# Kernel tuning notes

Hardware: AMD Instinct MI355X
Metric: run time of the kernel (lower is better)

The kernel has to match this reference:

```python
import jax, jax.numpy as jnp
import numpy as np

D_MODEL = 256  # out_channels + skip_channels
D_INNER = 512  # expand * d_model
D_STATE = 16
D_CONV = 4
DT_RANK = 16   # ceil(d_model / 16)


def setup_inputs() -> dict:
    key = jax.random.key(0)
    ks = jax.random.split(key, 16)
    s = 0.05
    inp = {
        "x": jax.random.normal(ks[0], (2, 256, 32, 32), jnp.float32),
        "skip": jax.random.normal(ks[1], (2, 128, 64, 64), jnp.float32),
        # ConvTranspose2d(in=256, out=128, k=2, s=2): torch weight (in, out, kH, kW)
        "up_w": jax.random.normal(ks[2], (256, 128, 2, 2), jnp.float32) * s,
        "up_b": jax.random.normal(ks[3], (128,), jnp.float32) * s,
        # Mamba params
        "in_proj_w": jax.random.normal(ks[4], (2 * D_INNER, D_MODEL), jnp.float32) * s,
        "conv1d_w": jax.random.normal(ks[5], (D_INNER, D_CONV), jnp.float32) * s,
        "conv1d_b": jax.random.normal(ks[6], (D_INNER,), jnp.float32) * s,
        "x_proj_w": jax.random.normal(ks[7], (DT_RANK + 2 * D_STATE, D_INNER), jnp.float32) * s,
        "dt_proj_w": jax.random.normal(ks[8], (D_INNER, DT_RANK), jnp.float32) * s,
        "dt_proj_b": jax.random.normal(ks[9], (D_INNER,), jnp.float32) * s,
        "A_log": jnp.log(jnp.tile(jnp.arange(1, D_STATE + 1, dtype=jnp.float32), (D_INNER, 1))),
        "D": jnp.ones((D_INNER,), jnp.float32),
        "out_proj_w": jax.random.normal(ks[10], (D_MODEL, D_INNER), jnp.float32) * s,
        # Conv2d(256 -> 128, k=3, pad=1) + BN affine
        "conv_w": jax.random.normal(ks[11], (128, 256, 3, 3), jnp.float32) * s,
        "conv_b": jax.random.normal(ks[12], (128,), jnp.float32) * s,
        "bn_gamma": jnp.ones((128,), jnp.float32),
        "bn_beta": jnp.zeros((128,), jnp.float32),
    }
    return inp


def _forward(x, skip, up_w, up_b, in_proj_w, conv1d_w, conv1d_b, x_proj_w,
             dt_proj_w, dt_proj_b, A_log, D, out_proj_w, conv_w, conv_b,
             bn_gamma, bn_beta):
    B, Cin, H, W = x.shape
    # --- ConvTranspose2d k=2, s=2: each input pixel expands to a 2x2 block ---
    up = jnp.einsum('bchw,coxy->bohxwy', x, up_w)  # (B, Cout, H, 2, W, 2)
    Cout = up_w.shape[1]
    up = up.reshape(B, Cout, 2 * H, 2 * W) + up_b[None, :, None, None]
    xc = jnp.concatenate([up, skip], axis=1)  # (B, d_model, 2H, 2W)
    _, d_model, H2, W2 = xc.shape
    L = H2 * W2
    seq = xc.reshape(B, d_model, L).transpose(0, 2, 1)  # (B, L, d_model)

    # --- Mamba block ---
    xz = seq @ in_proj_w.T  # (B, L, 2*d_inner)
    d_inner = in_proj_w.shape[0] // 2
    xi, z = xz[..., :d_inner], xz[..., d_inner:]
    # depthwise causal conv1d along L
    xt = xi.transpose(0, 2, 1)  # (B, d_inner, L)
    d_conv = conv1d_w.shape[-1]
    xt = jnp.pad(xt, ((0, 0), (0, 0), (d_conv - 1, 0)))
    xt = jax.lax.conv_general_dilated(
        xt, conv1d_w[:, None, :], (1,), 'VALID',
        dimension_numbers=('NCH', 'OIH', 'NCH'), feature_group_count=d_inner)
    xt = xt + conv1d_b[None, :, None]
    u = jax.nn.silu(xt.transpose(0, 2, 1))  # (B, L, d_inner)

    d_state = A_log.shape[1]
    dbc = u @ x_proj_w.T  # (B, L, dt_rank + 2*d_state)
    dt_rank = x_proj_w.shape[0] - 2 * d_state
    dt = jax.nn.softplus(dbc[..., :dt_rank] @ dt_proj_w.T + dt_proj_b)  # (B, L, d_inner)
    Bm = dbc[..., dt_rank:dt_rank + d_state]  # (B, L, d_state)
    Cm = dbc[..., dt_rank + d_state:]         # (B, L, d_state)
    A = -jnp.exp(A_log)                       # (d_inner, d_state)

    def step(h, inputs):
        dt_t, B_t, C_t, u_t = inputs  # (B,d_inner),(B,d_state),(B,d_state),(B,d_inner)
        dA = jnp.exp(dt_t[:, :, None] * A)  # (B, d_inner, d_state)
        h = dA * h + (dt_t * u_t)[:, :, None] * B_t[:, None, :]
        y_t = jnp.einsum('bdn,bn->bd', h, C_t)
        return h, y_t

    h0 = jnp.zeros((B, d_inner, d_state), seq.dtype)
    xs = (dt.transpose(1, 0, 2), Bm.transpose(1, 0, 2),
          Cm.transpose(1, 0, 2), u.transpose(1, 0, 2))
    _, ys = jax.lax.scan(step, h0, xs)  # ys: (L, B, d_inner)
    y = ys.transpose(1, 0, 2) + u * D
    y = y * jax.nn.silu(z)
    out = y @ out_proj_w.T  # (B, L, d_model)
    mam = out.transpose(0, 2, 1).reshape(B, d_model, H2, W2)

    # --- residual + Conv3x3 + BatchNorm (training stats) + GELU ---
    xr = xc + mam
    y2 = jax.lax.conv_general_dilated(
        xr, conv_w, (1, 1), ((1, 1), (1, 1)),
        dimension_numbers=('NCHW', 'OIHW', 'NCHW')) + conv_b[None, :, None, None]
    mu = y2.mean(axis=(0, 2, 3), keepdims=True)
    var = y2.var(axis=(0, 2, 3), keepdims=True)
    y2 = (y2 - mu) / jnp.sqrt(var + 1e-5) * bn_gamma[None, :, None, None] + bn_beta[None, :, None, None]
    return jax.nn.gelu(y2, approximate=False)


def reference(x, skip, up_w, up_b, in_proj_w, conv1d_w, conv1d_b, x_proj_w,
              dt_proj_w, dt_proj_b, A_log, D, out_proj_w, conv_w, conv_b,
              bn_gamma, bn_beta):
    return _forward(x, skip, up_w, up_b, in_proj_w, conv1d_w, conv1d_b,
                    x_proj_w, dt_proj_w, dt_proj_b, A_log, D, out_proj_w,
                    conv_w, conv_b, bn_gamma, bn_beta)
```

## Files before the change

kernel.cpp:

```cpp
#include <hip/hip_runtime.h>
#include <hip/hip_bf16.h>
#include <math.h>

typedef __hip_bfloat16 bf16;
typedef __attribute__((ext_vector_type(8))) short s8v;
typedef __attribute__((ext_vector_type(4))) float f4v;

#define NB 2
#define NT 8192
#define NSEG 128
#define SEGLEN 32


__device__ __forceinline__ short f2s(float x){
    bf16 t = __float2bfloat16(x);
    return *reinterpret_cast<short*>(&t);
}
__device__ __forceinline__ float s2f(short s){
    bf16 t = *reinterpret_cast<bf16*>(&s);
    return __bfloat162float(t);
}
__device__ __forceinline__ void powtree(float e1, float* a){
    a[0]=e1;      a[1]=a[0]*a[0];  a[2]=a[1]*a[0];  a[3]=a[1]*a[1];
    a[4]=a[3]*a[0]; a[5]=a[3]*a[1]; a[6]=a[3]*a[2]; a[7]=a[3]*a[3];
    a[8]=a[7]*a[0]; a[9]=a[7]*a[1]; a[10]=a[7]*a[2]; a[11]=a[7]*a[3];
    a[12]=a[7]*a[4]; a[13]=a[7]*a[5]; a[14]=a[7]*a[6]; a[15]=a[7]*a[7];
}

__global__ void k_prep3(const float* __restrict__ inw, const float* __restrict__ outw,
        const float* __restrict__ upw, const float* __restrict__ cvw,
        const float* __restrict__ xpw,
        short* inw_bf, short* outw_bf, short* upw_bf, short* cwt_bf,
        short* xw_bf, float* stats){
    int i = blockIdx.x*256 + threadIdx.x;
    if (i < 262144){ inw_bf[i] = f2s(inw[i]); }
    else if (i < 393216){ int j = i-262144; outw_bf[j] = f2s(outw[j]); }
    else if (i < 524288){
        int j = i-393216; int n = j >> 8, c = j & 255;
        upw_bf[j] = f2s(upw[c*512 + n]);
    }
    else if (i < 819200){
        int j = i-524288; int o = j / 2304, k = j % 2304;
        int p = k >> 8, c = k & 255;
        cwt_bf[j] = f2s(cvw[o*2304 + c*9 + p]);
    }
    else if (i < 851968){
        int j = i-819200; int r = j >> 9;
        xw_bf[j] = (r < 48) ? f2s(xpw[j]) : (short)0;
    }
    else if (i < 852224){ stats[i-851968] = 0.f; }
}

__global__ __launch_bounds__(256) void k_skipT(const float* __restrict__ skip,
        short* __restrict__ xc){
    __shared__ float tile[128][33];
    int bid = blockIdx.x;
    int b = bid >> 7, hw0 = (bid & 127)*32;
    int tid = threadIdx.x;
    int hwl = tid & 31, og = tid >> 5;
    #pragma unroll
    for (int it = 0; it < 16; ++it){
        int o = it*8 + og;
        tile[o][hwl] = skip[((size_t)(b*128 + o))*4096 + hw0 + hwl];
    }
    __syncthreads();
    int tl = tid >> 3, oc = (tid & 7)*16;
    int t = b*4096 + hw0 + tl;
    s8v v0, v1;
    #pragma unroll
    for (int q = 0; q < 8; ++q){
        v0[q] = f2s(tile[oc + q][tl]);
        v1[q] = f2s(tile[oc + 8 + q][tl]);
    }
    *(s8v*)(xc + (size_t)t*256 + 128 + oc)     = v0;
    *(s8v*)(xc + (size_t)t*256 + 128 + oc + 8) = v1;
}

__global__ __launch_bounds__(256) void k_xT(const float* __restrict__ x,
        short* __restrict__ xT){
    __shared__ float tile[32][257];
    int bid = blockIdx.x;
    int b = bid >> 5, p0 = (bid & 31)*32;
    int tid = threadIdx.x;
    int pl = tid & 31, cg = tid >> 5;
    #pragma unroll
    for (int it = 0; it < 32; ++it){
        int c = it*8 + cg;
        tile[pl][c] = x[((size_t)(b*256 + c))*1024 + p0 + pl];
    }
    __syncthreads();
    int pll = tid >> 3, cc = (tid & 7)*32;
    #pragma unroll
    for (int g = 0; g < 4; ++g){
        s8v v;
        #pragma unroll
        for (int q = 0; q < 8; ++q) v[q] = f2s(tile[pll][cc + g*8 + q]);
        *(s8v*)(xT + ((size_t)(b*1024 + p0 + pll))*256 + cc + g*8) = v;
    }
}

__device__ __forceinline__ s8v conv_loadA(const short* __restrict__ xr,
                                          int m, int kabs){
    int p = kabs >> 8, cin = kabs & 255;
    int dy = p/3 - 1, dx = p%3 - 1;
    int hw = m & 4095; int h = hw >> 6, w = hw & 63;
    int hh = h + dy, ww = w + dx;
    s8v v;
    if ((unsigned)hh < 64u && (unsigned)ww < 64u){
        v = *(const s8v*)(xr + (size_t)((m & ~4095) + (hh<<6) + ww)*256 + cin);
    } else {
        #pragma unroll
        for (int q = 0; q < 8; ++q) v[q] = 0;
    }
    return v;
}

template<int MODE>
__global__ __launch_bounds__(256) void k_mfma(const short* __restrict__ A, int lda,
        const short* __restrict__ B, int ldb, int K,
        void* __restrict__ Cd, int ldc, short* __restrict__ R,
        const float* __restrict__ Pf){
    __shared__ __align__(16) short As[128*72];
    __shared__ __align__(16) short Bs[64*72];
    const int tid = threadIdx.x;
    const int m0 = blockIdx.x*128, n0 = blockIdx.y*64;
    const int waveId = tid >> 6, lane = tid & 63;
    const int quad = lane >> 4, l15 = lane & 15;
    int kbase = 0;
    float* psum = nullptr;
    if (MODE == 3){
        kbase = blockIdx.z * 768;
        psum = (float*)Cd + (size_t)blockIdx.z * (8192*128);
    }
    f4v acc[2][4];
    #pragma unroll
    for (int a = 0; a < 2; ++a)
        #pragma unroll
        for (int b = 0; b < 4; ++b)
            acc[a][b] = (f4v){0.f,0.f,0.f,0.f};

    for (int k0 = 0; k0 < K; k0 += 64){
        __syncthreads();
        #pragma unroll
        for (int l = 0; l < 4; ++l){
            int c = tid + l*256;
            int row = c & 127, kq = c >> 7;
            s8v v;
            if (MODE == 3){
                v = conv_loadA(A, m0 + row, kbase + k0 + kq*8);
            } else {
                v = *(const s8v*)(A + (size_t)(m0+row)*lda + k0 + kq*8);
            }
            *(s8v*)&As[row*72 + kq*8] = v;
        }
        #pragma unroll
        for (int l = 0; l < 2; ++l){
            int c = tid + l*256;
            int n = c & 63, kq = c >> 6;
            *(s8v*)&Bs[n*72 + kq*8] =
                *(const s8v*)(B + (size_t)(n0+n)*ldb + kbase + k0 + kq*8);
        }
        __syncthreads();
        #pragma unroll
        for (int ks = 0; ks < 2; ++ks){
            s8v af[2], bfr[4];
            #pragma unroll
            for (int mi = 0; mi < 2; ++mi)
                af[mi] = *(s8v*)&As[(waveId*32 + mi*16 + l15)*72 + ks*32 + quad*8];
            #pragma unroll
            for (int ni = 0; ni < 4; ++ni)
                bfr[ni] = *(s8v*)&Bs[(ni*16 + l15)*72 + ks*32 + quad*8];
            #pragma unroll
            for (int mi = 0; mi < 2; ++mi)
                #pragma unroll
                for (int ni = 0; ni < 4; ++ni)
                    acc[mi][ni] = __builtin_amdgcn_mfma_f32_16x16x32_bf16(
                        af[mi], bfr[ni], acc[mi][ni], 0, 0, 0);
        }
    }
    #pragma unroll
    for (int mi = 0; mi < 2; ++mi){
        #pragma unroll
        for (int ni = 0; ni < 4; ++ni){
            int rowb = m0 + waveId*32 + mi*16 + quad*4;
            int col  = n0 + ni*16 + l15;
            #pragma unroll
            for (int r = 0; r < 4; ++r){
                int m = rowb + r;
                float v = acc[mi][ni][r];
                if (MODE == 2){
                    v += s2f(R[(size_t)m*ldc + col]);
                    ((short*)Cd)[(size_t)m*ldc + col] = f2s(v);
                } else if (MODE == 3){
                    psum[(size_t)m*128 + col] = v;
                } else if (MODE == 5){
                    int b = m >> 10, hp = (m & 1023) >> 5, wp = m & 31;
                    int o = col >> 2, ij = col & 3;
                    int h2 = 2*hp + (ij >> 1), w2 = 2*wp + (ij & 1);
                    int t = b*4096 + h2*64 + w2;
                    ((short*)Cd)[(size_t)t*256 + o] = f2s(v + Pf[o]);
                } else if (MODE == 6){
                    if (col < 512) ((short*)Cd)[(size_t)m*512 + col] = f2s(v);
                    else           R[(size_t)m*512 + col - 512]      = f2s(v);
                }
            }
        }
    }
}

__global__ __launch_bounds__(256) void k_reduce2(const float* __restrict__ psum,
        const float* __restrict__ cvb, float* __restrict__ y2,
        float* __restrict__ stats){
    __shared__ float ls[128], ls2[128];
    int tid = threadIdx.x;
    if (tid < 128){ ls[tid] = 0.f; ls2[tid] = 0.f; }
    __syncthreads();
    int base = blockIdx.x*4096;
    float lacc = 0.f, lacc2 = 0.f;
    int o = 0;
    #pragma unroll
    for (int it = 0; it < 16; ++it){
        int i = base + it*256 + tid;
        o = i & 127;
        float v = psum[i] + psum[i + 1048576] + psum[i + 2097152] + cvb[o];
        y2[i] = v;
        lacc += v; lacc2 += v*v;
    }
    atomicAdd(&ls[o], lacc);
    atomicAdd(&ls2[o], lacc2);
    __syncthreads();
    if (tid < 128){
        atomicAdd(&stats[tid], ls[tid]);
        atomicAdd(&stats[128 + tid], ls2[tid]);
    }
}

__global__ __launch_bounds__(256) void k_xproj32(const short* __restrict__ A,
        const short* __restrict__ B, float* __restrict__ dbc){
    __shared__ __align__(16) short As[2][32*72];
    __shared__ __align__(16) short Bs[2][64*72];
    const int tid = threadIdx.x;
    const int m0 = blockIdx.x*32;
    const int w = tid >> 6, lane = tid & 63;
    const int quad = lane >> 4, l15 = lane & 15;
    const int mi = w & 1, ni = w >> 1;
    const int arow = tid & 31, akq = tid >> 5;
    const int brow = tid & 63, bkq0 = tid >> 6, bkq1 = bkq0 + 4;

    s8v ra  = *(const s8v*)(A + (size_t)(m0+arow)*512 + akq*8);
    s8v rb0 = *(const s8v*)(B + (size_t)brow*512 + bkq0*8);
    s8v rb1 = *(const s8v*)(B + (size_t)brow*512 + bkq1*8);
    *(s8v*)&As[0][arow*72 + akq*8]  = ra;
    *(s8v*)&Bs[0][brow*72 + bkq0*8] = rb0;
    *(s8v*)&Bs[0][brow*72 + bkq1*8] = rb1;
    __syncthreads();

    f4v acc[2];
    acc[0] = (f4v){0.f,0.f,0.f,0.f};
    acc[1] = (f4v){0.f,0.f,0.f,0.f};
    int buf = 0;
    for (int kt = 0; kt < 8; ++kt){
        if (kt + 1 < 8){
            int k0 = (kt+1)*64;
            ra  = *(const s8v*)(A + (size_t)(m0+arow)*512 + k0 + akq*8);
            rb0 = *(const s8v*)(B + (size_t)brow*512 + k0 + bkq0*8);
            rb1 = *(const s8v*)(B + (size_t)brow*512 + k0 + bkq1*8);
        }
        #pragma unroll
        for (int ks = 0; ks < 2; ++ks){
            s8v af = *(s8v*)&As[buf][(mi*16 + l15)*72 + ks*32 + quad*8];
            #pragma unroll
            for (int nf = 0; nf < 2; ++nf){
                s8v bfv = *(s8v*)&Bs[buf][(ni*32 + nf*16 + l15)*72 + ks*32 + quad*8];
                acc[nf] = __builtin_amdgcn_mfma_f32_16x16x32_bf16(af, bfv, acc[nf], 0, 0, 0);
            }
        }
        if (kt + 1 < 8){
            __syncthreads();
            buf ^= 1;
            *(s8v*)&As[buf][arow*72 + akq*8]  = ra;
            *(s8v*)&Bs[buf][brow*72 + bkq0*8] = rb0;
            *(s8v*)&Bs[buf][brow*72 + bkq1*8] = rb1;
            __syncthreads();
        }
    }
    #pragma unroll
    for (int nf = 0; nf < 2; ++nf){
        int col = ni*32 + nf*16 + l15;
        if (col < 48){
            int rowb = m0 + mi*16 + quad*4;
            #pragma unroll
            for (int r = 0; r < 4; ++r)
                dbc[(size_t)(rowb+r)*48 + col] = acc[nf][r];
        }
    }
}

__global__ void k_conv1d(const short* __restrict__ xi, const float* __restrict__ cw,
                         const float* __restrict__ cb, short* __restrict__ u){
    int idx = blockIdx.x*256 + threadIdx.x;
    int t = idx >> 6; int dc = (idx & 63)*8; int l = t & 4095;
    s8v x0 = *(const s8v*)(xi + (size_t)t*512 + dc);
    s8v x1, x2, x3;
    #pragma unroll
    for (int q = 0; q < 8; ++q){ x1[q]=0; x2[q]=0; x3[q]=0; }
    if (l >= 1) x1 = *(const s8v*)(xi + (size_t)(t-1)*512 + dc);
    if (l >= 2) x2 = *(const s8v*)(xi + (size_t)(t-2)*512 + dc);
    if (l >= 3) x3 = *(const s8v*)(xi + (size_t)(t-3)*512 + dc);
    const float4* w4 = (const float4*)cw;
    s8v o;
    #pragma unroll
    for (int q = 0; q < 8; ++q){
        float4 w = w4[dc + q];
        float a = cb[dc+q] + s2f(x0[q])*w.w + s2f(x1[q])*w.z
                           + s2f(x2[q])*w.y + s2f(x3[q])*w.x;
        float s = a / (1.f + __expf(-a));
        o[q] = f2s(s);
    }
    *(s8v*)(u + (size_t)t*512 + dc) = o;
}

__global__ __launch_bounds__(256) void k_dtprep(const float* __restrict__ dbc,
        const float* __restrict__ dtw, const float* __restrict__ dtb,
        short* __restrict__ dtv){
    int base = blockIdx.x*256;
    int t = base >> 9;
    int d = (base & 511) + threadIdx.x;
    __shared__ float sD[16];
    if (threadIdx.x < 16) sD[threadIdx.x] = dbc[(size_t)t*48 + threadIdx.x];
    __syncthreads();
    const float4* w4 = (const float4*)(dtw + d*16);
    float4 wa = w4[0], wb = w4[1], wc = w4[2], wd = w4[3];
    float acc = dtb[d];
    acc += sD[0]*wa.x + sD[1]*wa.y + sD[2]*wa.z + sD[3]*wa.w;
    acc += sD[4]*wb.x + sD[5]*wb.y + sD[6]*wb.z + sD[7]*wb.w;
    acc += sD[8]*wc.x + sD[9]*wc.y + sD[10]*wc.z + sD[11]*wc.w;
    acc += sD[12]*wd.x + sD[13]*wd.y + sD[14]*wd.z + sD[15]*wd.w;
    float sp = (acc > 20.f) ? acc : log1pf(__expf(acc));
    dtv[(size_t)t*512 + d] = f2s(sp);
}

__global__ __launch_bounds__(256) void k_scanA4(const short* __restrict__ u,
        const short* __restrict__ dtv, const float* __restrict__ dbc,
        float* __restrict__ Sseg, short* __restrict__ Qb){
    int bid = blockIdx.x;
    int dh = bid & 1, s = (bid >> 1) & (NSEG-1), b = bid >> 8;
    int tid = threadIdx.x;
    int d = dh*256 + tid;
    int t0 = s*SEGLEN;
    __shared__ __align__(16) float4 sB4[SEGLEN][4];
    const float4* dbc4 = (const float4*)(dbc + (size_t)(b*4096 + t0)*48);
    for (int i = tid; i < SEGLEN*4; i += 256){
        int tl = i >> 2, g = i & 3;
        sB4[tl][g] = dbc4[tl*12 + 4 + g];
    }
    __syncthreads();
    float h[16];
    #pragma unroll
    for (int n = 0; n < 16; ++n) h[n] = 0.f;
    float S = 0.f;
    const short* up = u   + (size_t)(b*4096 + t0)*512 + d;
    const short* dp = dtv + (size_t)(b*4096 + t0)*512 + d;
    for (int tl = 0; tl < SEGLEN; ++tl){
        float dv = s2f(dp[(size_t)tl*512]);
        float e1 = __expf(-dv);
        float xv = dv * s2f(up[(size_t)tl*512]);
        float a[16];
        powtree(e1, a);
        float4 b0 = sB4[tl][0], b1 = sB4[tl][1], b2 = sB4[tl][2], b3 = sB4[tl][3];
        float B[16] = {b0.x,b0.y,b0.z,b0.w, b1.x,b1.y,b1.z,b1.w,
                       b2.x,b2.y,b2.z,b2.w, b3.x,b3.y,b3.z,b3.w};
        #pragma unroll
        for (int n = 0; n < 16; ++n)
            h[n] = a[n]*h[n] + xv*B[n];
        S += dv;
    }
    int ch = b*512 + d;
    Sseg[(size_t)ch*NSEG + s] = S;
    short* qp = Qb + ((size_t)ch*NSEG + s)*16;
    #pragma unroll
    for (int n = 0; n < 16; ++n) qp[n] = f2s(h[n]);
}

__global__ __launch_bounds__(256) void k_combine3(const float* __restrict__ Sseg,
        short* __restrict__ Qb){
    int gid = blockIdx.x*256 + threadIdx.x;
    int ch = gid >> 4, n = gid & 15;
    float np1 = (float)(n + 1);
    const float* sp = Sseg + (size_t)ch*NSEG;
    short* qp = Qb + (size_t)ch*NSEG*16 + n;
    float h = 0.f;
    #pragma unroll 4
    for (int s = 0; s < NSEG; ++s){
        float a = __expf(-np1 * sp[s]);
        float q = s2f(qp[(size_t)s*16]);
        float hin = h;
        h = a*h + q;
        qp[(size_t)s*16] = f2s(hin);
    }
}

__global__ __launch_bounds__(256) void k_scanC4(const short* __restrict__ u,
        const short* __restrict__ dtv, const float* __restrict__ dbc,
        short* __restrict__ zy, const float* __restrict__ Dpar,
        const short* __restrict__ Qb){
    int bid = blockIdx.x;
    int dh = bid & 1, s = (bid >> 1) & (NSEG-1), b = bid >> 8;
    int tid = threadIdx.x;
    int d = dh*256 + tid;
    int t0 = s*SEGLEN;
    __shared__ __align__(16) float4 sB4[SEGLEN][4], sC4[SEGLEN][4];
    const float4* dbc4 = (const float4*)(dbc + (size_t)(b*4096 + t0)*48);
    for (int i = tid; i < SEGLEN*8; i += 256){
        int tl = i >> 3, g = i & 7;
        if (g < 4) sB4[tl][g]   = dbc4[tl*12 + 4 + g];
        else       sC4[tl][g-4] = dbc4[tl*12 + 4 + g];
    }
    __syncthreads();
    float h[16];
    int ch = b*512 + d;
    const short* qp = Qb + ((size_t)ch*NSEG + s)*16;
    #pragma unroll
    for (int n = 0; n < 16; ++n) h[n] = s2f(qp[n]);
    float Dv = Dpar[d];
    const short* up = u   + (size_t)(b*4096 + t0)*512 + d;
    const short* dp = dtv + (size_t)(b*4096 + t0)*512 + d;
    short* zp       = zy  + (size_t)(b*4096 + t0)*512 + d;
    for (int tl = 0; tl < SEGLEN; ++tl){
        float dv = s2f(dp[(size_t)tl*512]);
        float e1 = __expf(-dv);
        float uv = s2f(up[(size_t)tl*512]);
        float xv = dv * uv;
        float a[16];
        powtree(e1, a);
        float4 b0 = sB4[tl][0], b1 = sB4[tl][1], b2 = sB4[tl][2], b3 = sB4[tl][3];
        float4 c0 = sC4[tl][0], c1 = sC4[tl][1], c2 = sC4[tl][2], c3 = sC4[tl][3];
        float B[16] = {b0.x,b0.y,b0.z,b0.w, b1.x,b1.y,b1.z,b1.w,
                       b2.x,b2.y,b2.z,b2.w, b3.x,b3.y,b3.z,b3.w};
        float C[16] = {c0.x,c0.y,c0.z,c0.w, c1.x,c1.y,c1.z,c1.w,
                       c2.x,c2.y,c2.z,c2.w, c3.x,c3.y,c3.z,c3.w};
        float y = 0.f;
        #pragma unroll
        for (int n = 0; n < 16; ++n){
            h[n] = a[n]*h[n] + xv*B[n];
            y += h[n]*C[n];
        }
        y += uv*Dv;
        float zv = s2f(zp[(size_t)tl*512]);
        float g = y * (zv / (1.f + __expf(-zv)));
        zp[(size_t)tl*512] = f2s(g);
    }
}

__global__ __launch_bounds__(256) void k_bngelu(const float* __restrict__ y2,
        const float* __restrict__ stats, const float* __restrict__ gam,
        const float* __restrict__ bet, float* __restrict__ out){
    __shared__ float tile[32][129];
    __shared__ float smu[128], sinv[128], sg[128], sb[128];
    int tid = threadIdx.x;
    int t0 = blockIdx.x*32;
    if (tid < 128){
        float s = stats[tid], s2 = stats[128 + tid];
        float mu = s * (1.f/8192.f);
        float var = s2 * (1.f/8192.f) - mu*mu;
        smu[tid] = mu; sinv[tid] = rsqrtf(var + 1e-5f);
        sg[tid] = gam[tid]; sb[tid] = bet[tid];
    }
    __syncthreads();
    for (int i = tid; i < 4096; i += 256){
        int r = i >> 7, c = i & 127;
        float v = y2[(size_t)(t0 + r)*128 + c];
        v = (v - smu[c])*sinv[c]*sg[c] + sb[c];
        tile[r][c] = 0.5f*v*(1.f + erff(v*0.7071067811865475f));
    }
    __syncthreads();
    for (int i = tid; i < 4096; i += 256){
        int o = i >> 5, q = i & 31;
        int t = t0 + q;
        int b = t >> 12, hw = t & 4095;
        out[((size_t)(b*128 + o))*4096 + hw] = tile[q][o];
    }
}

extern "C" void kernel_launch(void* const* d_in, const int* in_sizes, int n_in,
                              void* d_out, int out_size, void* d_ws, size_t ws_size,
                              hipStream_t stream){
    float* out = (float*)d_out;
    float* ws = (float*)d_ws;

    const float* x    = (const float*)d_in[0];
    const float* skip = (const float*)d_in[1];
    const float* upw  = (const float*)d_in[2];
    const float* upb  = (const float*)d_in[3];
    const float* inw  = (const float*)d_in[4];
    const float* c1w  = (const float*)d_in[5];
    const float* c1b  = (const float*)d_in[6];
    const float* xpw  = (const float*)d_in[7];
    const float* dtw  = (const float*)d_in[8];
    const float* dtb  = (const float*)d_in[9];
    const float* Dp   = (const float*)d_in[11];
    const float* outw = (const float*)d_in[12];
    const float* cvw  = (const float*)d_in[13];
    const float* cvb  = (const float*)d_in[14];
    const float* gam  = (const float*)d_in[15];
    const float* bet  = (const float*)d_in[16];

    float* stats = ws + 0;
    short* xc    = (short*)(ws + 256);
    short* xi    = (short*)(ws + 1048832);
    short* z     = (short*)(ws + 3145984);
    short* u     = (short*)(ws + 5243136);
    float* dbc   = ws + 7340288;
    float* Sseg  = ws + 7733504;
    short* Qb    = (short*)(ws + 7864576);
    short* xr    = (short*)(ws + 8913152);
    float* y2    = ws + 9961728;
    short* inw_bf  = (short*)(ws + 11010304);
    short* outw_bf = (short*)(ws + 11141376);
    short* upw_bf  = (short*)(ws + 11206912);
    short* cwt_bf  = (short*)(ws + 11272448);
    short* xw_bf   = (short*)(ws + 11419904);
    short* xT_bf   = (short*)(ws + 11436288);
    float* psum    = ws + 11698432;
    short* dtv     = (short*)(ws + 14844160);

    k_prep3<<<3329, 256, 0, stream>>>(inw, outw, upw, cvw, xpw,
            inw_bf, outw_bf, upw_bf, cwt_bf, xw_bf, stats);
    k_xT<<<64, 256, 0, stream>>>(x, xT_bf);
    k_skipT<<<256, 256, 0, stream>>>(skip, xc);
    k_mfma<5><<<dim3(16, 8), 256, 0, stream>>>(xT_bf, 256, upw_bf, 256, 256,
                                               xc, 256, nullptr, upb);
    k_mfma<6><<<dim3(64, 16), 256, 0, stream>>>(xc, 256, inw_bf, 256, 256,
                                                xi, 512, z, nullptr);
    k_conv1d<<<NT*64/256, 256, 0, stream>>>(xi, c1w, c1b, u);
    k_xproj32<<<256, 256, 0, stream>>>(u, xw_bf, dbc);
    k_dtprep<<<NT*512/256, 256, 0, stream>>>(dbc, dtw, dtb, dtv);
    k_scanA4<<<NB*NSEG*2, 256, 0, stream>>>(u, dtv, dbc, Sseg, Qb);
    k_combine3<<<64, 256, 0, stream>>>(Sseg, Qb);
    k_scanC4<<<NB*NSEG*2, 256, 0, stream>>>(u, dtv, dbc, z, Dp, Qb);
    k_mfma<2><<<dim3(64, 4), 256, 0, stream>>>(z, 512, outw_bf, 512, 512,
                                               xr, 256, xc, nullptr);
    k_mfma<3><<<dim3(64, 2, 3), 256, 0, stream>>>(xr, 256, cwt_bf, 2304, 768,
                                                  psum, 128, nullptr, nullptr);
    k_reduce2<<<256, 256, 0, stream>>>(psum, cvb, y2, stats);
    k_bngelu<<<256, 256, 0, stream>>>(y2, stats, gam, bet, out);
}
```

Measured before the change: 282.1 us.

## Fold dt_proj into x_proj weights and merge prep/transpose kernels

Precomputes the product of dt_proj and the dt rows of x_proj as extra bf16 weight rows, so the x-projection GEMM produces dt directly (grid widened to 9 column tiles) with bias and softplus applied in its epilogue. This removes the separate k_dtprep kernel. The weight-prep, x transpose and skip transpose kernels are also merged into one launch, cutting launch count. In exchange, dt is now computed in bf16 from a composed weight, which changes rounding, and the GEMM does 8x more MFMA work than the small 48-column projection it replaces.

```diff
diff --git a/kernel.cpp b/kernel.cpp
--- a/kernel.cpp
+++ b/kernel.cpp
@@ -27,75 +27,82 @@
     a[12]=a[7]*a[4]; a[13]=a[7]*a[5]; a[14]=a[7]*a[6]; a[15]=a[7]*a[7];
 }
 
-__global__ void k_prep3(const float* __restrict__ inw, const float* __restrict__ outw,
-        const float* __restrict__ upw, const float* __restrict__ cvw,
-        const float* __restrict__ xpw,
+__global__ __launch_bounds__(256) void k_prep4(const float* __restrict__ inw,
+        const float* __restrict__ outw, const float* __restrict__ upw,
+        const float* __restrict__ cvw, const float* __restrict__ xpw,
+        const float* __restrict__ dtw, const float* __restrict__ x,
+        const float* __restrict__ skip,
         short* inw_bf, short* outw_bf, short* upw_bf, short* cwt_bf,
-        short* xw_bf, float* stats){
-    int i = blockIdx.x*256 + threadIdx.x;
-    if (i < 262144){ inw_bf[i] = f2s(inw[i]); }
-    else if (i < 393216){ int j = i-262144; outw_bf[j] = f2s(outw[j]); }
-    else if (i < 524288){
-        int j = i-393216; int n = j >> 8, c = j & 255;
-        upw_bf[j] = f2s(upw[c*512 + n]);
-    }
-    else if (i < 819200){
-        int j = i-524288; int o = j / 2304, k = j % 2304;
-        int p = k >> 8, c = k & 255;
-        cwt_bf[j] = f2s(cvw[o*2304 + c*9 + p]);
-    }
-    else if (i < 851968){
-        int j = i-819200; int r = j >> 9;
-        xw_bf[j] = (r < 48) ? f2s(xpw[j]) : (short)0;
-    }
-    else if (i < 852224){ stats[i-851968] = 0.f; }
-}
-
-__global__ __launch_bounds__(256) void k_skipT(const float* __restrict__ skip,
-        short* __restrict__ xc){
-    __shared__ float tile[128][33];
-    int bid = blockIdx.x;
-    int b = bid >> 7, hw0 = (bid & 127)*32;
+        short* xwall_bf, short* xT_bf, short* xc, float* stats){
+    __shared__ float smem[32*257];
+    int bb = blockIdx.x;
     int tid = threadIdx.x;
-    int hwl = tid & 31, og = tid >> 5;
-    #pragma unroll
-    for (int it = 0; it < 16; ++it){
-        int o = it*8 + og;
-        tile[o][hwl] = skip[((size_t)(b*128 + o))*4096 + hw0 + hwl];
-    }
-    __syncthreads();
-    int tl = tid >> 3, oc = (tid & 7)*16;
-    int t = b*4096 + hw0 + tl;
-    s8v v0, v1;
-    #pragma unroll
-    for (int q = 0; q < 8; ++q){
-        v0[q] = f2s(tile[oc + q][tl]);
-        v1[q] = f2s(tile[oc + 8 + q][tl]);
-    }
-    *(s8v*)(xc + (size_t)t*256 + 128 + oc)     = v0;
-    *(s8v*)(xc + (size_t)t*256 + 128 + oc + 8) = v1;
-}
-
-__global__ __launch_bounds__(256) void k_xT(const float* __restrict__ x,
-        short* __restrict__ xT){
-    __shared__ float tile[32][257];
-    int bid = blockIdx.x;
-    int b = bid >> 5, p0 = (bid & 31)*32;
-    int tid = threadIdx.x;
-    int pl = tid & 31, cg = tid >> 5;
-    #pragma unroll
-    for (int it = 0; it < 32; ++it){
-        int c = it*8 + cg;
-        tile[pl][c] = x[((size_t)(b*256 + c))*1024 + p0 + pl];
-    }
-    __syncthreads();
-    int pll = tid >> 3, cc = (tid & 7)*32;
-    #pragma unroll
-    for (int g = 0; g < 4; ++g){
-        s8v v;
-        #pragma unroll
-        for (int q = 0; q < 8; ++q) v[q] = f2s(tile[pll][cc + g*8 + q]);
-        *(s8v*)(xT + ((size_t)(b*1024 + p0 + pll))*256 + cc + g*8) = v;
+    if (bb < 4353){
+        int i = bb*256 + tid;
+        if (i < 262144){ inw_bf[i] = f2s(inw[i]); }
+        else if (i < 393216){ int j = i-262144; outw_bf[j] = f2s(outw[j]); }
+        else if (i < 524288){
+            int j = i-393216; int n = j >> 8, c = j & 255;
+            upw_bf[j] = f2s(upw[c*512 + n]);
+        }
+        else if (i < 819200){
+            int j = i-524288; int o = j / 2304, k = j % 2304;
+            int p = k >> 8, c = k & 255;
+            cwt_bf[j] = f2s(cvw[o*2304 + c*9 + p]);
+        }
+        else if (i < 851968){
+            int j = i-819200; int r = j >> 9;
+            xwall_bf[j] = (r < 48) ? f2s(xpw[j]) : (short)0;
+        }
+        else if (i < 1114112){
+            int j = i-851968; int d = j >> 9, k = j & 511;
+            float acc = 0.f;
+            #pragma unroll
+            for (int q = 0; q < 16; ++q)
+                acc += dtw[d*16 + q]*xpw[q*512 + k];
+            xwall_bf[(size_t)(64 + d)*512 + k] = f2s(acc);
+        }
+        else if (i < 1114368){ stats[i-1114112] = 0.f; }
+    } else if (bb < 4417){
+        float (*tile)[257] = (float(*)[257])smem;
+        int bid = bb - 4353;
+        int b = bid >> 5, p0 = (bid & 31)*32;
+        int pl = tid & 31, cg = tid >> 5;
+        #pragma unroll
+        for (int it = 0; it < 32; ++it){
+            int c = it*8 + cg;
+            tile[pl][c] = x[((size_t)(b*256 + c))*1024 + p0 + pl];
+        }
+        __syncthreads();
+        int pll = tid >> 3, cc = (tid & 7)*32;
+        #pragma unroll
+        for (int g = 0; g < 4; ++g){
+            s8v v;
+            #pragma unroll
+            for (int q = 0; q < 8; ++q) v[q] = f2s(tile[pll][cc + g*8 + q]);
+            *(s8v*)(xT_bf + ((size_t)(b*1024 + p0 + pll))*256 + cc + g*8) = v;
+        }
+    } else {
+        float (*tile)[33] = (float(*)[33])smem;
+        int bid = bb - 4417;
+        int b = bid >> 7, hw0 = (bid & 127)*32;
+        int hwl = tid & 31, og = tid >> 5;
+        #pragma unroll
+        for (int it = 0; it < 16; ++it){
+            int o = it*8 + og;
+            tile[o][hwl] = skip[((size_t)(b*128 + o))*4096 + hw0 + hwl];
+        }
+        __syncthreads();
+        int tl = tid >> 3, oc = (tid & 7)*16;
+        int t = b*4096 + hw0 + tl;
+        s8v v0, v1;
+        #pragma unroll
+        for (int q = 0; q < 8; ++q){
+            v0[q] = f2s(tile[oc + q][tl]);
+            v1[q] = f2s(tile[oc + 8 + q][tl]);
+        }
+        *(s8v*)(xc + (size_t)t*256 + 128 + oc)     = v0;
+        *(s8v*)(xc + (size_t)t*256 + 128 + oc + 8) = v1;
     }
 }
 
@@ -235,12 +242,14 @@
     }
 }
 
-__global__ __launch_bounds__(256) void k_xproj32(const short* __restrict__ A,
-        const short* __restrict__ B, float* __restrict__ dbc){
+__global__ __launch_bounds__(256) void k_xprojdt(const short* __restrict__ A,
+        const short* __restrict__ B, const float* __restrict__ dtb,
+        float* __restrict__ dbc, short* __restrict__ dtv){
     __shared__ __align__(16) short As[2][32*72];
     __shared__ __align__(16) short Bs[2][64*72];
     const int tid = threadIdx.x;
     const int m0 = blockIdx.x*32;
+    const int n0 = blockIdx.y*64;
     const int w = tid >> 6, lane = tid & 63;
     const int quad = lane >> 4, l15 = lane & 15;
     const int mi = w & 1, ni = w >> 1;
@@ -248,8 +257,8 @@
     const int brow = tid & 63, bkq0 = tid >> 6, bkq1 = bkq0 + 4;
 
     s8v ra  = *(const s8v*)(A + (size_t)(m0+arow)*512 + akq*8);
-    s8v rb0 = *(const s8v*)(B + (size_t)brow*512 + bkq0*8);
-    s8v rb1 = *(const s8v*)(B + (size_t)brow*512 + bkq1*8);
+    s8v rb0 = *(const s8v*)(B + (size_t)(n0+brow)*512 + bkq0*8);
+    s8v rb1 = *(const s8v*)(B + (size_t)(n0+brow)*512 + bkq1*8);
     *(s8v*)&As[0][arow*72 + akq*8]  = ra;
     *(s8v*)&Bs[0][brow*72 + bkq0*8] = rb0;
     *(s8v*)&Bs[0][brow*72 + bkq1*8] = rb1;
@@ -263,8 +272,8 @@
         if (kt + 1 < 8){
             int k0 = (kt+1)*64;
             ra  = *(const s8v*)(A + (size_t)(m0+arow)*512 + k0 + akq*8);
-            rb0 = *(const s8v*)(B + (size_t)brow*512 + k0 + bkq0*8);
-            rb1 = *(const s8v*)(B + (size_t)brow*512 + k0 + bkq1*8);
+            rb0 = *(const s8v*)(B + (size_t)(n0+brow)*512 + k0 + bkq0*8);
+            rb1 = *(const s8v*)(B + (size_t)(n0+brow)*512 + k0 + bkq1*8);
         }
         #pragma unroll
         for (int ks = 0; ks < 2; ++ks){
@@ -286,12 +295,23 @@
     }
     #pragma unroll
     for (int nf = 0; nf < 2; ++nf){
-        int col = ni*32 + nf*16 + l15;
-        if (col < 48){
-            int rowb = m0 + mi*16 + quad*4;
-            #pragma unroll
-            for (int r = 0; r < 4; ++r)
-                dbc[(size_t)(rowb+r)*48 + col] = acc[nf][r];
+        int col = n0 + ni*32 + nf*16 + l15;
+        int rowb = m0 + mi*16 + quad*4;
+        if (blockIdx.y == 0){
+            if (col < 48){
+                #pragma unroll
+                for (int r = 0; r < 4; ++r)
+                    dbc[(size_t)(rowb+r)*48 + col] = acc[nf][r];
+            }
+        } else {
+            int d = col - 64;
+            float bias = dtb[d];
+            #pragma unroll
+            for (int r = 0; r < 4; ++r){
+                float a = acc[nf][r] + bias;
+                float sp = (a > 20.f) ? a : log1pf(__expf(a));
+                dtv[(size_t)(rowb+r)*512 + d] = f2s(sp);
+            }
         }
     }
 }
@@ -318,26 +338,6 @@
         o[q] = f2s(s);
     }
     *(s8v*)(u + (size_t)t*512 + dc) = o;
-}
-
-__global__ __launch_bounds__(256) void k_dtprep(const float* __restrict__ dbc,
-        const float* __restrict__ dtw, const float* __restrict__ dtb,
-        short* __restrict__ dtv){
-    int base = blockIdx.x*256;
-    int t = base >> 9;
-    int d = (base & 511) + threadIdx.x;
-    __shared__ float sD[16];
-    if (threadIdx.x < 16) sD[threadIdx.x] = dbc[(size_t)t*48 + threadIdx.x];
-    __syncthreads();
-    const float4* w4 = (const float4*)(dtw + d*16);
-    float4 wa = w4[0], wb = w4[1], wc = w4[2], wd = w4[3];
-    float acc = dtb[d];
-    acc += sD[0]*wa.x + sD[1]*wa.y + sD[2]*wa.z + sD[3]*wa.w;
-    acc += sD[4]*wb.x + sD[5]*wb.y + sD[6]*wb.z + sD[7]*wb.w;
-    acc += sD[8]*wc.x + sD[9]*wc.y + sD[10]*wc.z + sD[11]*wc.w;
-    acc += sD[12]*wd.x + sD[13]*wd.y + sD[14]*wd.z + sD[15]*wd.w;
-    float sp = (acc > 20.f) ? acc : log1pf(__expf(acc));
-    dtv[(size_t)t*512 + d] = f2s(sp);
 }
 
 __global__ __launch_bounds__(256) void k_scanA4(const short* __restrict__ u,
@@ -519,22 +519,19 @@
     short* outw_bf = (short*)(ws + 11141376);
     short* upw_bf  = (short*)(ws + 11206912);
     short* cwt_bf  = (short*)(ws + 11272448);
-    short* xw_bf   = (short*)(ws + 11419904);
     short* xT_bf   = (short*)(ws + 11436288);
     float* psum    = ws + 11698432;
     short* dtv     = (short*)(ws + 14844160);
-
-    k_prep3<<<3329, 256, 0, stream>>>(inw, outw, upw, cvw, xpw,
-            inw_bf, outw_bf, upw_bf, cwt_bf, xw_bf, stats);
-    k_xT<<<64, 256, 0, stream>>>(x, xT_bf);
-    k_skipT<<<256, 256, 0, stream>>>(skip, xc);
+    short* xwall_bf= (short*)(ws + 16941312);
+
+    k_prep4<<<4673, 256, 0, stream>>>(inw, outw, upw, cvw, xpw, dtw, x, skip,
+            inw_bf, outw_bf, upw_bf, cwt_bf, xwall_bf, xT_bf, xc, stats);
     k_mfma<5><<<dim3(16, 8), 256, 0, stream>>>(xT_bf, 256, upw_bf, 256, 256,
                                                xc, 256, nullptr, upb);
     k_mfma<6><<<dim3(64, 16), 256, 0, stream>>>(xc, 256, inw_bf, 256, 256,
                                                 xi, 512, z, nullptr);
     k_conv1d<<<NT*64/256, 256, 0, stream>>>(xi, c1w, c1b, u);
-    k_xproj32<<<256, 256, 0, stream>>>(u, xw_bf, dbc);
-    k_dtprep<<<NT*512/256, 256, 0, stream>>>(dbc, dtw, dtb, dtv);
+    k_xprojdt<<<dim3(256, 9), 256, 0, stream>>>(u, xwall_bf, dtb, dbc, dtv);
     k_scanA4<<<NB*NSEG*2, 256, 0, stream>>>(u, dtv, dbc, Sseg, Qb);
     k_combine3<<<64, 256, 0, stream>>>(Sseg, Qb);
     k_scanC4<<<NB*NSEG*2, 256, 0, stream>>>(u, dtv, dbc, z, Dp, Qb);
```

After: 284.7 us. About the same (+0.9%).
